# Optimization experiments

Hardware: AMD Instinct MI355X
Metric: run time of the kernel (lower is better)

The kernel has to match this reference:

```python
import jax, jax.numpy as jnp
import numpy as np


def setup_inputs() -> dict:
    key = jax.random.key(0)
    k1, k2 = jax.random.split(key)
    B, N, M, D = 4, 1024, 1024, 64
    traj1 = jax.random.normal(k1, (B, N, D), dtype=jnp.float32)
    traj2 = jax.random.normal(k2, (B, M, D), dtype=jnp.float32)
    return {"traj1": traj1, "traj2": traj2}


def reference(traj1, traj2):
    # Pairwise squared Euclidean distances: [B, N, M]
    # Faithful to sum((traj1[:, :, None] - traj2[:, None, :])**2, -1)
    diff = traj1[:, :, None, :] - traj2[:, None, :, :]  # [B, N, M, D]
    return jnp.sum(jnp.square(diff), axis=-1)
```

## Files before the change

kernel.cpp:

```cpp
#include <hip/hip_runtime.h>


#define B_ 4
#define N_ 1024
#define M_ 1024
#define D_ 64
#define BN 128
#define BM 128

typedef __attribute__((ext_vector_type(8))) __fp16 f16x8;
typedef __attribute__((ext_vector_type(2))) __fp16 f16x2;
typedef __attribute__((ext_vector_type(4))) float f32x4;

union F16x8 {
  f16x8 v;
  f16x2 h[4];
};

__device__ __forceinline__ f16x8 load_frag8(const float* __restrict__ p) {
  float4 v0 = *reinterpret_cast<const float4*>(p);
  float4 v1 = *reinterpret_cast<const float4*>(p + 4);
  F16x8 r;
  r.h[0] = __builtin_amdgcn_cvt_pkrtz(v0.x, v0.y);
  r.h[1] = __builtin_amdgcn_cvt_pkrtz(v0.z, v0.w);
  r.h[2] = __builtin_amdgcn_cvt_pkrtz(v1.x, v1.y);
  r.h[3] = __builtin_amdgcn_cvt_pkrtz(v1.z, v1.w);
  return r.v;
}

__global__ __launch_bounds__(512, 4)
void dist2_mfma(const float* __restrict__ A, const float* __restrict__ Bm,
                float* __restrict__ out) {
  __shared__ float naS[BN];
  __shared__ float nbS[BM];

  const int tid = threadIdx.x;
  const int b  = blockIdx.z;
  const int n0 = blockIdx.y * BN;
  const int m0 = blockIdx.x * BM;

  const float* Ab = A  + (size_t)b * N_ * D_;
  const float* Bb = Bm + (size_t)b * M_ * D_;

  if (tid < BN + BM) {
    const float* p = (tid < BN) ? (Ab + (size_t)(n0 + tid) * D_)
                                : (Bb + (size_t)(m0 + tid - BN) * D_);
    float s = 0.f;
    #pragma unroll
    for (int k4 = 0; k4 < D_ / 4; ++k4) {
      float4 v = *reinterpret_cast<const float4*>(p + k4 * 4);
      s = fmaf(v.x, v.x, s);
      s = fmaf(v.y, v.y, s);
      s = fmaf(v.z, v.z, s);
      s = fmaf(v.w, v.w, s);
    }
    if (tid < BN) naS[tid] = s; else nbS[tid - BN] = s;
  }

  const int wid  = tid >> 6;
  const int lane = tid & 63;
  const int wrow = wid >> 2;
  const int wcol = wid & 3;
  const int lr    = lane & 15;
  const int kbase = (lane >> 4) * 8;

  const float* Arow = Ab + (size_t)(n0 + wrow * 64 + lr) * D_;
  const float* Brow = Bb + (size_t)(m0 + wcol * 32 + lr) * D_;

  f32x4 acc[4][2];
  #pragma unroll
  for (int i = 0; i < 4; ++i)
    #pragma unroll
    for (int j = 0; j < 2; ++j) acc[i][j] = (f32x4){0.f, 0.f, 0.f, 0.f};

  #pragma unroll
  for (int ks = 0; ks < 2; ++ks) {
    const int k = ks * 32 + kbase;
    f16x8 af[4], bf[2];
    #pragma unroll
    for (int i = 0; i < 4; ++i) af[i] = load_frag8(Arow + (size_t)i * 16 * D_ + k);
    #pragma unroll
    for (int j = 0; j < 2; ++j) bf[j] = load_frag8(Brow + (size_t)j * 16 * D_ + k);
    #pragma unroll
    for (int i = 0; i < 4; ++i)
      #pragma unroll
      for (int j = 0; j < 2; ++j)
        acc[i][j] = __builtin_amdgcn_mfma_f32_16x16x32_f16(af[i], bf[j], acc[i][j], 0, 0, 0);
  }

  __syncthreads();

  const int colA  = lane & 15;
  const int rbase = (lane >> 4) * 4;

  #pragma unroll
  for (int i = 0; i < 4; ++i) {
    #pragma unroll
    for (int j = 0; j < 2; ++j) {
      const int   col = wcol * 32 + j * 16 + colA;
      const float nb  = nbS[col];
      #pragma unroll
      for (int q = 0; q < 4; ++q) {
        const int row = wrow * 64 + i * 16 + rbase + q;
        const float na = naS[row];
        out[((size_t)b * N_ + n0 + row) * M_ + m0 + col] =
            fmaf(-2.f, acc[i][j][q], na + nb);
      }
    }
  }
}

extern "C" void kernel_launch(void* const* d_in, const int* in_sizes, int n_in,
                              void* d_out, int out_size, void* d_ws, size_t ws_size,
                              hipStream_t stream) {
  const float* A  = (const float*)d_in[0];
  const float* Bm = (const float*)d_in[1];
  float* out = (float*)d_out;
  dim3 grid(M_ / BM, N_ / BN, B_);
  dist2_mfma<<<grid, dim3(512), 0, stream>>>(A, Bm, out);
}
```

Baseline: 16.89 us.

## Swap MFMA operands to emit float4 row-contiguous stores and shrink tile to 64x128

Swaps the A and B operands of the MFMA so each lane's four accumulator values lie along the M dimension of the output. The epilogue can then write them as one float4 store per fragment instead of four scalar stores with a row stride. The block tile also shrinks from 128x128 to 64x128 with 256 threads and four waves of 32x64 each, which doubles the grid. The output is a 16 MB write-bound stream, so the change targets store efficiency, at the cost of more blocks and more redundant norm computation.

```diff
diff --git a/kernel.cpp b/kernel.cpp
--- a/kernel.cpp
+++ b/kernel.cpp
@@ -5,7 +5,7 @@
 #define N_ 1024
 #define M_ 1024
 #define D_ 64
-#define BN 128
+#define BN 64
 #define BM 128
 
 typedef __attribute__((ext_vector_type(8))) __fp16 f16x8;
@@ -28,7 +28,7 @@
   return r.v;
 }
 
-__global__ __launch_bounds__(512, 4)
+__global__ __launch_bounds__(256, 2)
 void dist2_mfma(const float* __restrict__ A, const float* __restrict__ Bm,
                 float* __restrict__ out) {
   __shared__ float naS[BN];
@@ -59,53 +59,55 @@
 
   const int wid  = tid >> 6;
   const int lane = tid & 63;
-  const int wrow = wid >> 2;
-  const int wcol = wid & 3;
-  const int lr    = lane & 15;
-  const int kbase = (lane >> 4) * 8;
+  const int wn = wid >> 1;
+  const int wm = wid & 1;
+  const int lr = lane & 15;
+  const int kb = (lane >> 4) * 8;
 
-  const float* Arow = Ab + (size_t)(n0 + wrow * 64 + lr) * D_;
-  const float* Brow = Bb + (size_t)(m0 + wcol * 32 + lr) * D_;
+  const float* An = Ab + (size_t)(n0 + wn * 32 + lr) * D_;
+  const float* Bn = Bb + (size_t)(m0 + wm * 64 + lr) * D_;
 
-  f32x4 acc[4][2];
+  f32x4 acc[2][4];
   #pragma unroll
-  for (int i = 0; i < 4; ++i)
+  for (int i = 0; i < 2; ++i)
     #pragma unroll
-    for (int j = 0; j < 2; ++j) acc[i][j] = (f32x4){0.f, 0.f, 0.f, 0.f};
+    for (int j = 0; j < 4; ++j) acc[i][j] = (f32x4){0.f, 0.f, 0.f, 0.f};
 
   #pragma unroll
   for (int ks = 0; ks < 2; ++ks) {
-    const int k = ks * 32 + kbase;
-    f16x8 af[4], bf[2];
+    const int k = ks * 32 + kb;
+    f16x8 af[2], bf[4];
     #pragma unroll
-    for (int i = 0; i < 4; ++i) af[i] = load_frag8(Arow + (size_t)i * 16 * D_ + k);
+    for (int nf = 0; nf < 2; ++nf) af[nf] = load_frag8(An + (size_t)nf * 16 * D_ + k);
     #pragma unroll
-    for (int j = 0; j < 2; ++j) bf[j] = load_frag8(Brow + (size_t)j * 16 * D_ + k);
+    for (int mf = 0; mf < 4; ++mf) bf[mf] = load_frag8(Bn + (size_t)mf * 16 * D_ + k);
     #pragma unroll
-    for (int i = 0; i < 4; ++i)
+    for (int nf = 0; nf < 2; ++nf)
       #pragma unroll
-      for (int j = 0; j < 2; ++j)
-        acc[i][j] = __builtin_amdgcn_mfma_f32_16x16x32_f16(af[i], bf[j], acc[i][j], 0, 0, 0);
+      for (int mf = 0; mf < 4; ++mf)
+        acc[nf][mf] = __builtin_amdgcn_mfma_f32_16x16x32_f16(bf[mf], af[nf], acc[nf][mf], 0, 0, 0);
   }
 
   __syncthreads();
 
-  const int colA  = lane & 15;
-  const int rbase = (lane >> 4) * 4;
+  const int mg = (lane >> 4) * 4;
 
   #pragma unroll
-  for (int i = 0; i < 4; ++i) {
+  for (int nf = 0; nf < 2; ++nf) {
+    const int nloc = wn * 32 + nf * 16 + (lane & 15);
+    const float na = naS[nloc];
+    float* orow = out + ((size_t)b * N_ + n0 + nloc) * M_ + m0;
     #pragma unroll
-    for (int j = 0; j < 2; ++j) {
-      const int   col = wcol * 32 + j * 16 + colA;
-      const float nb  = nbS[col];
-      #pragma unroll
-      for (int q = 0; q < 4; ++q) {
-        const int row = wrow * 64 + i * 16 + rbase + q;
-        const float na = naS[row];
-        out[((size_t)b * N_ + n0 + row) * M_ + m0 + col] =
-            fmaf(-2.f, acc[i][j][q], na + nb);
-      }
+    for (int mf = 0; mf < 4; ++mf) {
+      const int mloc = wm * 64 + mf * 16 + mg;
+      float4 nb = *reinterpret_cast<const float4*>(&nbS[mloc]);
+      f32x4 a = acc[nf][mf];
+      float4 r;
+      r.x = fmaf(-2.f, a[0], na + nb.x);
+      r.y = fmaf(-2.f, a[1], na + nb.y);
+      r.z = fmaf(-2.f, a[2], na + nb.z);
+      r.w = fmaf(-2.f, a[3], na + nb.w);
+      *reinterpret_cast<float4*>(orow + mloc) = r;
     }
   }
 }
@@ -117,5 +119,5 @@
   const float* Bm = (const float*)d_in[1];
   float* out = (float*)d_out;
   dim3 grid(M_ / BM, N_ / BN, B_);
-  dist2_mfma<<<grid, dim3(512), 0, stream>>>(A, Bm, out);
+  dist2_mfma<<<grid, dim3(256), 0, stream>>>(A, Bm, out);
 }
```

Result: slower. 17.70 us (+4.8%).
